# Performance work log

Hardware: AMD Instinct MI355X
Metric: run time of the kernel (lower is better)

Reference implementation:

```python
import jax, jax.numpy as jnp
import numpy as np

MUL = 32
HEAD_DIM = 16
CLIP = 5.0
EPS = 1e-6
INV_SQRTD = 1.0 / np.sqrt(HEAD_DIM)
ENV_BLOCKS = (1, 3)          # 0e, 1o
TP_BLOCKS = (1, 1, 3, 3)     # 0e(0x0), 0e(1x1), 1o(0x1), 1o(1x0)


def so3_layernorm(x, g, block_dims):
    """x: [..., MUL, D]; per-irrep-block RMS norm over (mul, components), affine scale g [MUL, n_blocks]."""
    out, i = [], 0
    for b, d in enumerate(block_dims):
        blk = x[..., i:i + d]
        n = jnp.sqrt(jnp.mean(blk * blk, axis=(-2, -1), keepdims=True) + EPS)
        out.append(blk / n * g[:, b][:, None])
        i += d
    return jnp.concatenate(out, axis=-1)


def scatter_softmax(logits, seg, num_segments):
    """softmax over edges grouped by destination node. logits [E, M]."""
    m = jax.ops.segment_max(logits, seg, num_segments=num_segments)
    e = jnp.exp(logits - m[seg])
    d = jax.ops.segment_sum(e, seg, num_segments=num_segments)
    return e / d[seg]


def setup_inputs() -> dict:
    key = jax.random.key(0)
    ks = jax.random.split(key, 16)
    N, E, LAT, NODE_DIM, COND, HID = 16384, 262144, 64, 64, 32, 128
    sc = lambda f: f ** -0.5
    return {
        "node_attrs": jax.random.normal(ks[0], (N, NODE_DIM), jnp.float32),
        "scalar_state": jax.random.normal(ks[1], (E, LAT), jnp.float32),
        "equiv_state": jax.random.normal(ks[2], (E, MUL, 4), jnp.float32),
        "edge_conditioning": jax.random.normal(ks[3], (E, COND), jnp.float32),
        "residual_update_coeff": jax.random.uniform(ks[4], (1,), jnp.float32),
        "W_env1": jax.random.normal(ks[5], (LAT + COND, HID), jnp.float32) * sc(LAT + COND),
        "b_env1": jnp.zeros((HID,), jnp.float32),
        "W_env2": jax.random.normal(ks[6], (HID, MUL * 2), jnp.float32) * sc(HID),
        "Wq": jax.random.normal(ks[7], (NODE_DIM, MUL * HEAD_DIM), jnp.float32) * sc(NODE_DIM),
        "Wk": jax.random.normal(ks[8], (LAT, MUL * HEAD_DIM), jnp.float32) * sc(LAT),
        "g_env": jnp.ones((MUL, 2), jnp.float32),
        "g_tp": jnp.ones((MUL, 4), jnp.float32),
        "Wp1": jax.random.normal(ks[9], (MUL * 2 + COND, HID), jnp.float32) * sc(MUL * 2 + COND),
        "bp1": jnp.zeros((HID,), jnp.float32),
        "Wp2": jax.random.normal(ks[10], (HID, LAT + MUL * 4), jnp.float32) * sc(HID),
        "edge_src": jax.random.randint(ks[11], (E,), 0, N),
    }


def reference(node_attrs, scalar_state, equiv_state, edge_conditioning,
              residual_update_coeff, W_env1, b_env1, W_env2, Wq, Wk,
              g_env, g_tp, Wp1, bp1, Wp2, edge_src):
    N = node_attrs.shape[0]
    E = scalar_state.shape[0]
    LAT = scalar_state.shape[1]

    # --- env_embed_mlp: scalar MLP -> per-(mul, irrep-block) gates on equiv state ---
    x = jnp.concatenate([scalar_state, edge_conditioning], axis=-1)
    h = jax.nn.silu(x @ W_env1 + b_env1)
    w = (h @ W_env2).reshape(E, MUL, 2)                    # [E, mul, 2 blocks]
    w_exp = jnp.repeat(w, np.array(ENV_BLOCKS), axis=-1, total_repeat_length=4)
    env_edges = equiv_state * w_exp                        # [E, mul, 4]

    # --- attention: edge-gathered query, clipped logits, scatter softmax ---
    Q = (node_attrs[edge_src] @ Wq).reshape(E, MUL, HEAD_DIM)
    K = (scalar_state @ Wk).reshape(E, MUL, HEAD_DIM)
    logits = jnp.einsum('emd,emd->em', Q, K) * INV_SQRTD
    logits = jnp.clip(logits, -CLIP, CLIP)
    attn = scatter_softmax(logits, edge_src, N)            # [E, mul]
    env_edges = env_edges * attn[..., None]

    # --- scatter-sum to nodes, SO3 layernorm, gather back ---
    env_nodes = jax.ops.segment_sum(env_edges, edge_src, num_segments=N)  # [N, mul, 4]
    env_nodes = so3_layernorm(env_nodes, g_env, ENV_BLOCKS)
    edge_local_env = env_nodes[edge_src]                   # [E, mul, 4]

    # --- Contracter, uuu mode, instructions: 0x0->0, 1x1->0, 0x1->1, 1x0->1 ---
    s1, v1 = equiv_state[..., 0], equiv_state[..., 1:4]
    s2, v2 = edge_local_env[..., 0], edge_local_env[..., 1:4]
    o0a = s1 * s2                                          # 0e
    o0b = jnp.einsum('emi,emi->em', v1, v2) / np.sqrt(3.0) # 0e (CG of 1x1->0)
    o1a = s1[..., None] * v2                               # 1o
    o1b = v1 * s2[..., None]                               # 1o
    tp_out = jnp.concatenate([o0a[..., None], o0b[..., None], o1a, o1b], axis=-1)  # [E, mul, 8]
    tp_out = so3_layernorm(tp_out, g_tp, TP_BLOCKS)

    # --- projection: scalar MLP -> new scalar latent + per-path weights mixing equiv blocks ---
    scalars = tp_out[..., :2].reshape(E, MUL * 2)
    xp = jnp.concatenate([scalars, edge_conditioning], axis=-1)
    hp = jax.nn.silu(xp @ Wp1 + bp1)
    op = hp @ Wp2
    new_scalar = op[:, :LAT]
    pw = op[:, LAT:].reshape(E, MUL, 4)
    new_s = pw[..., 0] * tp_out[..., 0] + pw[..., 1] * tp_out[..., 1]
    new_v = pw[..., 2:3] * tp_out[..., 2:5] + pw[..., 3:4] * tp_out[..., 5:8]
    new_equiv = jnp.concatenate([new_s[..., None], new_v], axis=-1)  # [E, mul, 4]

    # --- residual streams ---
    c_old = jax.lax.rsqrt(residual_update_coeff ** 2 + 1.0)
    c_new = residual_update_coeff * c_old
    scalar_out = c_old * scalar_state + c_new * new_scalar
    equiv_out = c_old * equiv_state + c_new * new_equiv
    return scalar_out, equiv_out
```

## Files before the change

### kernel.cpp

```cpp
#include <hip/hip_runtime.h>
#include <math.h>

#define EPSF 1e-6f
#define STX 100
#define STH 132

__device__ __forceinline__ float silu_f(float x){ return x * (1.0f/(1.0f + __expf(-x))); }

__global__ __launch_bounds__(256) void k_qnode(
    const float* __restrict__ na, const float* __restrict__ Wq,
    float* __restrict__ qn)
{
  __shared__ float At[64*16];
  const int nb = blockIdx.x * 16;
  const int t = threadIdx.x;
  for (int f = t; f < 16*64; f += 256){ int n = f>>6, i = f&63; At[i*16+n] = na[(size_t)(nb+n)*64 + i]; }
  __syncthreads();
  float acc0[16], acc1[16];
#pragma unroll
  for (int n=0;n<16;n++){ acc0[n]=0.f; acc1[n]=0.f; }
  for (int i=0;i<64;i++){
    float w0 = Wq[(size_t)i*512 + t];
    float w1 = Wq[(size_t)i*512 + t + 256];
#pragma unroll
    for (int n=0;n<16;n++){ float a = At[i*16+n]; acc0[n] = fmaf(a,w0,acc0[n]); acc1[n] = fmaf(a,w1,acc1[n]); }
  }
#pragma unroll
  for (int n=0;n<16;n++){
    qn[(size_t)(nb+n)*512 + t]       = acc0[n];
    qn[(size_t)(nb+n)*512 + t + 256] = acc1[n];
  }
}

__global__ __launch_bounds__(256,4) void k_edge1(
    const float* __restrict__ ssi, const float* __restrict__ cond,
    const float* __restrict__ equiv, const int* __restrict__ esrc,
    const float* __restrict__ W1, const float* __restrict__ b1,
    const float* __restrict__ W2, const float* __restrict__ Wk,
    const float* __restrict__ qn,
    float* __restrict__ denom, float* __restrict__ num)
{
  __shared__ float Xs[32*STX];
  __shared__ float Hs[32*STH];
  __shared__ float lg[32*32];
  __shared__ int src_l[32];
  const int e0 = blockIdx.x * 32;
  const int t = threadIdx.x;
  const int r0 = (t>>5)*4;

  if (t < 32) src_l[t] = esrc[e0+t];
  for (int f=t; f<512; f+=256){ int r=f>>4, q=(f&15)*4;
    *(float4*)(Xs + r*STX + q) = *(const float4*)(ssi + (size_t)(e0+r)*64 + q); }
  { int f=t; int r=f>>3, q=(f&7)*4;
    *(float4*)(Xs + r*STX + 64 + q) = *(const float4*)(cond + (size_t)(e0+r)*32 + q); }
  __syncthreads();

  {
    const int c0 = (t&31)*4;
    float acc[4][4] = {};
    for (int i0=0;i0<96;i0+=4){
      float4 wv[4], xv[4];
#pragma unroll
      for (int k=0;k<4;k++) wv[k] = *(const float4*)(W1 + (size_t)(i0+k)*128 + c0);
#pragma unroll
      for (int rr=0;rr<4;rr++) xv[rr] = *(const float4*)(Xs + (r0+rr)*STX + i0);
#pragma unroll
      for (int rr=0;rr<4;rr++){
        const float xs[4] = {xv[rr].x,xv[rr].y,xv[rr].z,xv[rr].w};
#pragma unroll
        for (int k=0;k<4;k++){
          acc[rr][0] = fmaf(xs[k], wv[k].x, acc[rr][0]);
          acc[rr][1] = fmaf(xs[k], wv[k].y, acc[rr][1]);
          acc[rr][2] = fmaf(xs[k], wv[k].z, acc[rr][2]);
          acc[rr][3] = fmaf(xs[k], wv[k].w, acc[rr][3]);
        }
      }
    }
    const float4 bb = *(const float4*)(b1 + c0);
#pragma unroll
    for (int rr=0;rr<4;rr++){
      float4 h;
      h.x = silu_f(acc[rr][0]+bb.x); h.y = silu_f(acc[rr][1]+bb.y);
      h.z = silu_f(acc[rr][2]+bb.z); h.w = silu_f(acc[rr][3]+bb.w);
      *(float4*)(Hs + (r0+rr)*STH + c0) = h;
    }
  }
  __syncthreads();

  float wacc[4][2] = {};
  {
    const int c0 = (t&31)*2;
    for (int j0=0;j0<128;j0+=4){
      float2 w2[4]; float4 hv[4];
#pragma unroll
      for (int k=0;k<4;k++) w2[k] = *(const float2*)(W2 + (size_t)(j0+k)*64 + c0);
#pragma unroll
      for (int rr=0;rr<4;rr++) hv[rr] = *(const float4*)(Hs + (r0+rr)*STH + j0);
#pragma unroll
      for (int rr=0;rr<4;rr++){
        const float hs[4] = {hv[rr].x,hv[rr].y,hv[rr].z,hv[rr].w};
#pragma unroll
        for (int k=0;k<4;k++){
          wacc[rr][0] = fmaf(hs[k], w2[k].x, wacc[rr][0]);
          wacc[rr][1] = fmaf(hs[k], w2[k].y, wacc[rr][1]);
        }
      }
    }
  }
  __syncthreads();
  float* wl = Hs;
  {
    const int c0 = (t&31)*2;
#pragma unroll
    for (int rr=0;rr<4;rr++)
      *(float2*)(wl + (r0+rr)*66 + c0) = make_float2(wacc[rr][0], wacc[rr][1]);
  }

  for (int it=0; it<4; it++){
    const int c0k = (t&31)*4 + it*128;
    float acc[4][4] = {};
    for (int i0=0;i0<64;i0+=4){
      float4 wv[4], xv[4];
#pragma unroll
      for (int k=0;k<4;k++) wv[k] = *(const float4*)(Wk + (size_t)(i0+k)*512 + c0k);
#pragma unroll
      for (int rr=0;rr<4;rr++) xv[rr] = *(const float4*)(Xs + (r0+rr)*STX + i0);
#pragma unroll
      for (int rr=0;rr<4;rr++){
        const float xs[4] = {xv[rr].x,xv[rr].y,xv[rr].z,xv[rr].w};
#pragma unroll
        for (int k=0;k<4;k++){
          acc[rr][0] = fmaf(xs[k], wv[k].x, acc[rr][0]);
          acc[rr][1] = fmaf(xs[k], wv[k].y, acc[rr][1]);
          acc[rr][2] = fmaf(xs[k], wv[k].z, acc[rr][2]);
          acc[rr][3] = fmaf(xs[k], wv[k].w, acc[rr][3]);
        }
      }
    }
    const int m = ((t&31)>>2) + it*8;
#pragma unroll
    for (int rr=0;rr<4;rr++){
      const float4 q = *(const float4*)(qn + (size_t)src_l[r0+rr]*512 + c0k);
      float p = acc[rr][0]*q.x + acc[rr][1]*q.y + acc[rr][2]*q.z + acc[rr][3]*q.w;
      p += __shfl_xor(p, 1);
      p += __shfl_xor(p, 2);
      if ((t&3)==0) lg[(r0+rr)*32 + m] = p;
    }
  }
  __syncthreads();

  for (int f=t; f<1024; f+=256){
    int r=f>>5, m=f&31;
    float l = lg[f] * 0.25f;
    l = fminf(5.0f, fmaxf(-5.0f, l));
    float el = __expf(l);
    lg[f] = el;
    atomicAdd(denom + (size_t)src_l[r]*32 + m, el);
  }
  __syncthreads();

  for (int f=t; f<1024; f+=256){
    int r=f>>5, m=f&31;
    const float el = lg[r*32+m];
    const float w0 = wl[r*66 + 2*m]   * el;
    const float w1 = wl[r*66 + 2*m+1] * el;
    const float4 ev = *(const float4*)(equiv + ((size_t)(e0+r)*32 + m)*4);
    float* np = num + (size_t)src_l[r]*128 + 4*m;
    atomicAdd(np+0, w0*ev.x);
    atomicAdd(np+1, w1*ev.y);
    atomicAdd(np+2, w1*ev.z);
    atomicAdd(np+3, w1*ev.w);
  }
}

__global__ __launch_bounds__(128) void k_dnorm(
    float* __restrict__ num, const float* __restrict__ denom,
    const float* __restrict__ g_env)
{
  __shared__ float red[128];
  __shared__ float inv0s, inv1s;
  const int n = blockIdx.x, t = threadIdx.x;
  const int m = t>>2, c = t&3;
  const float d = denom[(size_t)n*32+m];
  const float x = (d > 0.0f) ? num[(size_t)n*128+t]/d : 0.0f;
  red[t] = x*x;
  __syncthreads();
  if (t < 32){
    float p0 = red[4*t];
    float p1 = red[4*t+1]+red[4*t+2]+red[4*t+3];
#pragma unroll
    for (int k=1;k<32;k<<=1){ p0 += __shfl_xor(p0,k); p1 += __shfl_xor(p1,k); }
    if (t==0){ inv0s = 1.0f/sqrtf(p0*(1.0f/32.0f) + EPSF); inv1s = 1.0f/sqrtf(p1*(1.0f/96.0f) + EPSF); }
  }
  __syncthreads();
  const float g = g_env[m*2 + (c?1:0)];
  num[(size_t)n*128+t] = x * (c ? inv1s : inv0s) * g;
}

__global__ __launch_bounds__(256,3) void k_edge2(
    const float* __restrict__ ssi, const float* __restrict__ cond,
    const float* __restrict__ equiv, const int* __restrict__ esrc,
    const float* __restrict__ envn, const float* __restrict__ g_tp,
    const float* __restrict__ Wp1, const float* __restrict__ bp1,
    const float* __restrict__ Wp2, const float* __restrict__ ruc,
    float* __restrict__ outs, float* __restrict__ oute)
{
  __shared__ float envl[32*STH];
  __shared__ float Xp[32*STX];
  __shared__ float Hp[32*STH];
  __shared__ float inv_l[32*4];
  __shared__ int src_l[32];
  const int e0 = blockIdx.x * 32;
  const int t = threadIdx.x;
  const int r0 = (t>>5)*4;
  if (t < 32) src_l[t] = esrc[e0+t];
  __syncthreads();
  for (int f=t; f<1024; f+=256){ int r=f>>5, q=(f&31)*4;
    *(float4*)(envl + r*STH + q) = *(const float4*)(envn + (size_t)src_l[r]*128 + q); }
  { int f=t; int r=f>>3, q=(f&7)*4;
    *(float4*)(Xp + r*STX + 64 + q) = *(const float4*)(cond + (size_t)(e0+r)*32 + q); }
  __syncthreads();

  {
    const int r = t>>3, sub = t&7;
    float ss0=0,ss1=0,ss2=0,ss3=0;
#pragma unroll
    for (int mm=0;mm<4;mm++){
      const int m = sub*4+mm;
      const float4 e4 = *(const float4*)(equiv + ((size_t)(e0+r)*32 + m)*4);
      const float4 n4 = *(const float4*)(envl + r*STH + 4*m);
      const float tp0 = e4.x*n4.x;
      const float dv  = e4.y*n4.y + e4.z*n4.z + e4.w*n4.w;
      const float tp1 = dv*0.5773502691896258f;
      ss0 += tp0*tp0;
      ss1 += tp1*tp1;
      ss2 += e4.x*e4.x*(n4.y*n4.y + n4.z*n4.z + n4.w*n4.w);
      ss3 += n4.x*n4.x*(e4.y*e4.y + e4.z*e4.z + e4.w*e4.w);
    }
#pragma unroll
    for (int k=1;k<8;k<<=1){
      ss0 += __shfl_xor(ss0,k); ss1 += __shfl_xor(ss1,k);
      ss2 += __shfl_xor(ss2,k); ss3 += __shfl_xor(ss3,k);
    }
    if (sub == 0){
      inv_l[r*4+0] = 1.0f/sqrtf(ss0*(1.0f/32.0f) + EPSF);
      inv_l[r*4+1] = 1.0f/sqrtf(ss1*(1.0f/32.0f) + EPSF);
      inv_l[r*4+2] = 1.0f/sqrtf(ss2*(1.0f/96.0f) + EPSF);
      inv_l[r*4+3] = 1.0f/sqrtf(ss3*(1.0f/96.0f) + EPSF);
    }
  }
  __syncthreads();

  for (int f=t; f<2048; f+=256){
    const int r = f>>6, col = f&63, m = col>>1;
    const float4 e4 = *(const float4*)(equiv + ((size_t)(e0+r)*32 + m)*4);
    const float4 n4 = *(const float4*)(envl + r*STH + 4*m);
    float v;
    if (col & 1)
      v = (e4.y*n4.y + e4.z*n4.z + e4.w*n4.w)*0.5773502691896258f * inv_l[r*4+1] * g_tp[m*4+1];
    else
      v = e4.x*n4.x * inv_l[r*4+0] * g_tp[m*4+0];
    Xp[r*STX + col] = v;
  }
  __syncthreads();

  {
    const int c0 = (t&31)*4;
    float acc[4][4] = {};
    for (int i0=0;i0<96;i0+=4){
      float4 wv[4], xv[4];
#pragma unroll
      for (int k=0;k<4;k++) wv[k] = *(const float4*)(Wp1 + (size_t)(i0+k)*128 + c0);
#pragma unroll
      for (int rr=0;rr<4;rr++) xv[rr] = *(const float4*)(Xp + (r0+rr)*STX + i0);
#pragma unroll
      for (int rr=0;rr<4;rr++){
        const float xs[4] = {xv[rr].x,xv[rr].y,xv[rr].z,xv[rr].w};
#pragma unroll
        for (int k=0;k<4;k++){
          acc[rr][0] = fmaf(xs[k], wv[k].x, acc[rr][0]);
          acc[rr][1] = fmaf(xs[k], wv[k].y, acc[rr][1]);
          acc[rr][2] = fmaf(xs[k], wv[k].z, acc[rr][2]);
          acc[rr][3] = fmaf(xs[k], wv[k].w, acc[rr][3]);
        }
      }
    }
    const float4 bb = *(const float4*)(bp1 + c0);
#pragma unroll
    for (int rr=0;rr<4;rr++){
      float4 h;
      h.x = silu_f(acc[rr][0]+bb.x); h.y = silu_f(acc[rr][1]+bb.y);
      h.z = silu_f(acc[rr][2]+bb.z); h.w = silu_f(acc[rr][3]+bb.w);
      *(float4*)(Hp + (r0+rr)*STH + c0) = h;
    }
  }
  __syncthreads();

  const float rv = ruc[0];
  const float c_old = 1.0f/sqrtf(rv*rv + 1.0f);
  const float c_new = rv * c_old;

  {
    const int c0 = (t&31)*2;
    float acc[4][2] = {};
    for (int j0=0;j0<128;j0+=4){
      float2 w2[4]; float4 hv[4];
#pragma unroll
      for (int k=0;k<4;k++) w2[k] = *(const float2*)(Wp2 + (size_t)(j0+k)*192 + c0);
#pragma unroll
      for (int rr=0;rr<4;rr++) hv[rr] = *(const float4*)(Hp + (r0+rr)*STH + j0);
#pragma unroll
      for (int rr=0;rr<4;rr++){
        const float hs[4] = {hv[rr].x,hv[rr].y,hv[rr].z,hv[rr].w};
#pragma unroll
        for (int k=0;k<4;k++){
          acc[rr][0] = fmaf(hs[k], w2[k].x, acc[rr][0]);
          acc[rr][1] = fmaf(hs[k], w2[k].y, acc[rr][1]);
        }
      }
    }
#pragma unroll
    for (int rr=0;rr<4;rr++){
      const size_t e = (size_t)(e0+r0+rr);
      const float2 s2 = *(const float2*)(ssi + e*64 + c0);
      float2 o2; o2.x = c_old*s2.x + c_new*acc[rr][0]; o2.y = c_old*s2.y + c_new*acc[rr][1];
      *(float2*)(outs + e*64 + c0) = o2;
    }
  }

  {
    const int m = t&31;
    float acc[4][4] = {};
    for (int j0=0;j0<128;j0+=4){
      float4 w4[4]; float4 hv[4];
#pragma unroll
      for (int k=0;k<4;k++) w4[k] = *(const float4*)(Wp2 + (size_t)(j0+k)*192 + 64 + 4*m);
#pragma unroll
      for (int rr=0;rr<4;rr++) hv[rr] = *(const float4*)(Hp + (r0+rr)*STH + j0);
#pragma unroll
      for (int rr=0;rr<4;rr++){
        const float hs[4] = {hv[rr].x,hv[rr].y,hv[rr].z,hv[rr].w};
#pragma unroll
        for (int k=0;k<4;k++){
          acc[rr][0] = fmaf(hs[k], w4[k].x, acc[rr][0]);
          acc[rr][1] = fmaf(hs[k], w4[k].y, acc[rr][1]);
          acc[rr][2] = fmaf(hs[k], w4[k].z, acc[rr][2]);
          acc[rr][3] = fmaf(hs[k], w4[k].w, acc[rr][3]);
        }
      }
    }
    const float g2 = g_tp[m*4+2], g3 = g_tp[m*4+3];
#pragma unroll
    for (int rr=0;rr<4;rr++){
      const int r = r0+rr;
      const size_t e = (size_t)(e0+r);
      const float4 e4 = *(const float4*)(equiv + (e*32 + m)*4);
      const float4 n4 = *(const float4*)(envl + r*STH + 4*m);
      const float tpn0 = Xp[r*STX + 2*m];
      const float tpn1 = Xp[r*STX + 2*m+1];
      const float a2 = acc[rr][2]*inv_l[r*4+2]*g2;
      const float a3 = acc[rr][3]*inv_l[r*4+3]*g3;
      float4 o;
      o.x = c_old*e4.x + c_new*(acc[rr][0]*tpn0 + acc[rr][1]*tpn1);
      o.y = c_old*e4.y + c_new*(a2*(e4.x*n4.y) + a3*(e4.y*n4.x));
      o.z = c_old*e4.z + c_new*(a2*(e4.x*n4.z) + a3*(e4.z*n4.x));
      o.w = c_old*e4.w + c_new*(a2*(e4.x*n4.w) + a3*(e4.w*n4.x));
      *(float4*)(oute + e*128 + 4*m) = o;
    }
  }
}

extern "C" void kernel_launch(void* const* d_in, const int* in_sizes, int n_in,
                              void* d_out, int out_size, void* d_ws, size_t ws_size,
                              hipStream_t stream)
{
  const float* na   = (const float*)d_in[0];
  const float* ssi  = (const float*)d_in[1];
  const float* eqv  = (const float*)d_in[2];
  const float* cond = (const float*)d_in[3];
  const float* ruc  = (const float*)d_in[4];
  const float* W1   = (const float*)d_in[5];
  const float* b1   = (const float*)d_in[6];
  const float* W2   = (const float*)d_in[7];
  const float* Wq   = (const float*)d_in[8];
  const float* Wk   = (const float*)d_in[9];
  const float* ge   = (const float*)d_in[10];
  const float* gt   = (const float*)d_in[11];
  const float* Wp1  = (const float*)d_in[12];
  const float* bp1  = (const float*)d_in[13];
  const float* Wp2  = (const float*)d_in[14];
  const int*   esrc = (const int*)d_in[15];

  const int N = in_sizes[0] / 64;
  const int E = in_sizes[1] / 64;

  float* denom = (float*)d_ws;
  float* num   = denom + (size_t)N*32;
  float* qn    = num   + (size_t)N*128;
  float* outs  = (float*)d_out;
  float* oute  = outs + (size_t)E*64;

  hipMemsetAsync(d_ws, 0, (size_t)N*160*sizeof(float), stream);
  k_qnode<<<N/16, 256, 0, stream>>>(na, Wq, qn);
  k_edge1<<<E/32, 256, 0, stream>>>(ssi, cond, eqv, esrc, W1, b1, W2, Wk, qn, denom, num);
  k_dnorm<<<N, 128, 0, stream>>>(num, denom, ge);
  k_edge2<<<E/32, 256, 0, stream>>>(ssi, cond, eqv, esrc, num, gt, Wp1, bp1, Wp2, ruc, outs, oute);
}
```

Measured before the change: 1.393 ms.

## Replace atomic scatter-softmax aggregation with CSR segmented reduction by source node

Builds a CSR index of edges grouped by source node (histogram, single-block scan, atomic scatter into a permutation) and changes the first edge kernel to write per-edge exp-logits and weighted values to a workspace buffer. A new per-node kernel then gathers each node's edges to form the softmax denominator, numerator and layer norm without float atomics. The aim is to remove heavy atomic contention on node accumulators. In exchange it adds several small launches, a serial single-block scan, a large per-edge intermediate buffer and irregular gathers, and it falls back to the old atomic path when the workspace is too small.

Measured after the change: 1.372 ms. Within noise of the previous version (-1.6%).

```diff
diff --git a/kernel.cpp b/kernel.cpp
--- a/kernel.cpp
+++ b/kernel.cpp
@@ -32,7 +32,209 @@
   }
 }
 
+__global__ __launch_bounds__(256) void k_hist(
+    const int* __restrict__ esrc, int E, int* __restrict__ cnt)
+{
+  int i = blockIdx.x*256 + threadIdx.x;
+  if (i < E) atomicAdd(cnt + esrc[i], 1);
+}
+
+__global__ __launch_bounds__(1024) void k_scan(
+    int* __restrict__ cnt_cur, int N, int* __restrict__ off)
+{
+  __shared__ int part[1024];
+  const int t = threadIdx.x;
+  const int ipt = (N + 1023) >> 10;
+  int s = 0;
+  for (int k=0;k<ipt;k++){ int i = t*ipt + k; if (i < N) s += cnt_cur[i]; }
+  part[t] = s;
+  __syncthreads();
+  for (int d=1; d<1024; d<<=1){
+    int v = (t >= d) ? part[t-d] : 0;
+    __syncthreads();
+    part[t] += v;
+    __syncthreads();
+  }
+  int run = (t==0) ? 0 : part[t-1];
+  for (int k=0;k<ipt;k++){
+    int i = t*ipt + k;
+    if (i < N){ int c = cnt_cur[i]; off[i] = run; cnt_cur[i] = run; run += c; }
+  }
+  if (t == 1023) off[N] = part[1023];
+}
+
+__global__ __launch_bounds__(256) void k_scatter(
+    const int* __restrict__ esrc, int E, int* __restrict__ cur, int* __restrict__ perm)
+{
+  int i = blockIdx.x*256 + threadIdx.x;
+  if (i < E){ int p = atomicAdd(cur + esrc[i], 1); perm[p] = i; }
+}
+
 __global__ __launch_bounds__(256,4) void k_edge1(
+    const float* __restrict__ ssi, const float* __restrict__ cond,
+    const int* __restrict__ esrc,
+    const float* __restrict__ W1, const float* __restrict__ b1,
+    const float* __restrict__ W2, const float* __restrict__ Wk,
+    const float* __restrict__ qn,
+    float* __restrict__ elw)
+{
+  __shared__ float Xs[32*STX];
+  __shared__ float Hs[32*STH];
+  __shared__ float lg[32*32];
+  __shared__ int src_l[32];
+  const int e0 = blockIdx.x * 32;
+  const int t = threadIdx.x;
+  const int r0 = (t>>5)*4;
+
+  if (t < 32) src_l[t] = esrc[e0+t];
+  for (int f=t; f<512; f+=256){ int r=f>>4, q=(f&15)*4;
+    *(float4*)(Xs + r*STX + q) = *(const float4*)(ssi + (size_t)(e0+r)*64 + q); }
+  { int f=t; int r=f>>3, q=(f&7)*4;
+    *(float4*)(Xs + r*STX + 64 + q) = *(const float4*)(cond + (size_t)(e0+r)*32 + q); }
+  __syncthreads();
+
+  {
+    const int c0 = (t&31)*4;
+    float acc[4][4] = {};
+    for (int i0=0;i0<96;i0+=4){
+      float4 wv[4], xv[4];
+#pragma unroll
+      for (int k=0;k<4;k++) wv[k] = *(const float4*)(W1 + (size_t)(i0+k)*128 + c0);
+#pragma unroll
+      for (int rr=0;rr<4;rr++) xv[rr] = *(const float4*)(Xs + (r0+rr)*STX + i0);
+#pragma unroll
+      for (int rr=0;rr<4;rr++){
+        const float xs[4] = {xv[rr].x,xv[rr].y,xv[rr].z,xv[rr].w};
+#pragma unroll
+        for (int k=0;k<4;k++){
+          acc[rr][0] = fmaf(xs[k], wv[k].x, acc[rr][0]);
+          acc[rr][1] = fmaf(xs[k], wv[k].y, acc[rr][1]);
+          acc[rr][2] = fmaf(xs[k], wv[k].z, acc[rr][2]);
+          acc[rr][3] = fmaf(xs[k], wv[k].w, acc[rr][3]);
+        }
+      }
+    }
+    const float4 bb = *(const float4*)(b1 + c0);
+#pragma unroll
+    for (int rr=0;rr<4;rr++){
+      float4 h;
+      h.x = silu_f(acc[rr][0]+bb.x); h.y = silu_f(acc[rr][1]+bb.y);
+      h.z = silu_f(acc[rr][2]+bb.z); h.w = silu_f(acc[rr][3]+bb.w);
+      *(float4*)(Hs + (r0+rr)*STH + c0) = h;
+    }
+  }
+  __syncthreads();
+
+  float wacc[4][2] = {};
+  {
+    const int c0 = (t&31)*2;
+    for (int j0=0;j0<128;j0+=4){
+      float2 w2[4]; float4 hv[4];
+#pragma unroll
+      for (int k=0;k<4;k++) w2[k] = *(const float2*)(W2 + (size_t)(j0+k)*64 + c0);
+#pragma unroll
+      for (int rr=0;rr<4;rr++) hv[rr] = *(const float4*)(Hs + (r0+rr)*STH + j0);
+#pragma unroll
+      for (int rr=0;rr<4;rr++){
+        const float hs[4] = {hv[rr].x,hv[rr].y,hv[rr].z,hv[rr].w};
+#pragma unroll
+        for (int k=0;k<4;k++){
+          wacc[rr][0] = fmaf(hs[k], w2[k].x, wacc[rr][0]);
+          wacc[rr][1] = fmaf(hs[k], w2[k].y, wacc[rr][1]);
+        }
+      }
+    }
+  }
+  __syncthreads();
+  float* wl = Hs;
+  {
+    const int c0 = (t&31)*2;
+#pragma unroll
+    for (int rr=0;rr<4;rr++)
+      *(float2*)(wl + (r0+rr)*66 + c0) = make_float2(wacc[rr][0], wacc[rr][1]);
+  }
+
+  for (int it=0; it<4; it++){
+    const int c0k = (t&31)*4 + it*128;
+    float acc[4][4] = {};
+    for (int i0=0;i0<64;i0+=4){
+      float4 wv[4], xv[4];
+#pragma unroll
+      for (int k=0;k<4;k++) wv[k] = *(const float4*)(Wk + (size_t)(i0+k)*512 + c0k);
+#pragma unroll
+      for (int rr=0;rr<4;rr++) xv[rr] = *(const float4*)(Xs + (r0+rr)*STX + i0);
+#pragma unroll
+      for (int rr=0;rr<4;rr++){
+        const float xs[4] = {xv[rr].x,xv[rr].y,xv[rr].z,xv[rr].w};
+#pragma unroll
+        for (int k=0;k<4;k++){
+          acc[rr][0] = fmaf(xs[k], wv[k].x, acc[rr][0]);
+          acc[rr][1] = fmaf(xs[k], wv[k].y, acc[rr][1]);
+          acc[rr][2] = fmaf(xs[k], wv[k].z, acc[rr][2]);
+          acc[rr][3] = fmaf(xs[k], wv[k].w, acc[rr][3]);
+        }
+      }
+    }
+    const int m = ((t&31)>>2) + it*8;
+#pragma unroll
+    for (int rr=0;rr<4;rr++){
+      const float4 q = *(const float4*)(qn + (size_t)src_l[r0+rr]*512 + c0k);
+      float p = acc[rr][0]*q.x + acc[rr][1]*q.y + acc[rr][2]*q.z + acc[rr][3]*q.w;
+      p += __shfl_xor(p, 1);
+      p += __shfl_xor(p, 2);
+      if ((t&3)==0) lg[(r0+rr)*32 + m] = p;
+    }
+  }
+  __syncthreads();
+
+  for (int f=t; f<1024; f+=256){
+    int r=f>>5, m=f&31;
+    float l = lg[f] * 0.25f;
+    l = fminf(5.0f, fmaxf(-5.0f, l));
+    const float el = __expf(l);
+    const size_t b = (size_t)(e0+r)*96;
+    elw[b + m]      = el;
+    elw[b + 32 + m] = el * wl[r*66 + 2*m];
+    elw[b + 64 + m] = el * wl[r*66 + 2*m+1];
+  }
+}
+
+__global__ __launch_bounds__(128) void k_env(
+    const float* __restrict__ elw, const float* __restrict__ equiv,
+    const int* __restrict__ perm, const int* __restrict__ off,
+    const float* __restrict__ g_env, float* __restrict__ envn)
+{
+  __shared__ float red[128];
+  __shared__ float inv0s, inv1s;
+  const int n = blockIdx.x, t = threadIdx.x;
+  const int m = t>>2, c = t&3;
+  const int j0 = off[n], j1 = off[n+1];
+  float den = 0.f, acc = 0.f;
+  for (int j=j0; j<j1; j++){
+    const int pe = perm[j];
+    const size_t b = (size_t)pe*96;
+    const float el = elw[b + m];
+    const float a  = elw[b + (c ? 64 : 32) + m];
+    const float ev = equiv[((size_t)pe*32 + m)*4 + c];
+    den += el;
+    acc = fmaf(a, ev, acc);
+  }
+  const float x = (den > 0.f) ? acc/den : 0.f;
+  red[t] = x*x;
+  __syncthreads();
+  if (t < 32){
+    float p0 = red[4*t];
+    float p1 = red[4*t+1]+red[4*t+2]+red[4*t+3];
+#pragma unroll
+    for (int k=1;k<32;k<<=1){ p0 += __shfl_xor(p0,k); p1 += __shfl_xor(p1,k); }
+    if (t==0){ inv0s = 1.0f/sqrtf(p0*(1.0f/32.0f) + EPSF); inv1s = 1.0f/sqrtf(p1*(1.0f/96.0f) + EPSF); }
+  }
+  __syncthreads();
+  const float g = g_env[m*2 + (c?1:0)];
+  envn[(size_t)n*128 + t] = x * (c ? inv1s : inv0s) * g;
+}
+
+__global__ __launch_bounds__(256,4) void k_edge1_atm(
     const float* __restrict__ ssi, const float* __restrict__ cond,
     const float* __restrict__ equiv, const int* __restrict__ esrc,
     const float* __restrict__ W1, const float* __restrict__ b1,
@@ -394,15 +596,37 @@
   const int N = in_sizes[0] / 64;
   const int E = in_sizes[1] / 64;
 
-  float* denom = (float*)d_ws;
-  float* num   = denom + (size_t)N*32;
-  float* qn    = num   + (size_t)N*128;
   float* outs  = (float*)d_out;
   float* oute  = outs + (size_t)E*64;
 
-  hipMemsetAsync(d_ws, 0, (size_t)N*160*sizeof(float), stream);
-  k_qnode<<<N/16, 256, 0, stream>>>(na, Wq, qn);
-  k_edge1<<<E/32, 256, 0, stream>>>(ssi, cond, eqv, esrc, W1, b1, W2, Wk, qn, denom, num);
-  k_dnorm<<<N, 128, 0, stream>>>(num, denom, ge);
-  k_edge2<<<E/32, 256, 0, stream>>>(ssi, cond, eqv, esrc, num, gt, Wp1, bp1, Wp2, ruc, outs, oute);
-}
+  const size_t need = ((size_t)N*128 + (size_t)N*512 + (size_t)E*96) * sizeof(float)
+                    + ((size_t)2*N + 1 + (size_t)E) * sizeof(int);
+
+  if (ws_size >= need) {
+    float* envn = (float*)d_ws;
+    float* qn   = envn + (size_t)N*128;
+    float* elw  = qn   + (size_t)N*512;
+    int*   off  = (int*)(elw + (size_t)E*96);
+    int*   cur  = off + (N + 1);
+    int*   perm = cur + N;
+
+    hipMemsetAsync(cur, 0, (size_t)N*sizeof(int), stream);
+    k_qnode  <<<N/16, 256, 0, stream>>>(na, Wq, qn);
+    k_hist   <<<(E+255)/256, 256, 0, stream>>>(esrc, E, cur);
+    k_scan   <<<1, 1024, 0, stream>>>(cur, N, off);
+    k_scatter<<<(E+255)/256, 256, 0, stream>>>(esrc, E, cur, perm);
+    k_edge1  <<<E/32, 256, 0, stream>>>(ssi, cond, esrc, W1, b1, W2, Wk, qn, elw);
+    k_env    <<<N, 128, 0, stream>>>(elw, eqv, perm, off, ge, envn);
+    k_edge2  <<<E/32, 256, 0, stream>>>(ssi, cond, eqv, esrc, envn, gt, Wp1, bp1, Wp2, ruc, outs, oute);
+  } else {
+    float* denom = (float*)d_ws;
+    float* num   = denom + (size_t)N*32;
+    float* qn    = num   + (size_t)N*128;
+
+    hipMemsetAsync(d_ws, 0, (size_t)N*160*sizeof(float), stream);
+    k_qnode    <<<N/16, 256, 0, stream>>>(na, Wq, qn);
+    k_edge1_atm<<<E/32, 256, 0, stream>>>(ssi, cond, eqv, esrc, W1, b1, W2, Wk, qn, denom, num);
+    k_dnorm    <<<N, 128, 0, stream>>>(num, denom, ge);
+    k_edge2    <<<E/32, 256, 0, stream>>>(ssi, cond, eqv, esrc, num, gt, Wp1, bp1, Wp2, ruc, outs, oute);
+  }
+}
```
